# Kernel optimization log

Hardware: AMD Instinct MI355X
Metric: run time of the kernel (lower is better)

The kernel has to match this reference:

```python
import jax, jax.numpy as jnp
import numpy as np

LEAKY_SLOPE = 0.2
MASK_VAL = -9e15


def setup_inputs() -> dict:
    key = jax.random.key(0)
    k1, k2, k3, k4, k5, k6 = jax.random.split(key, 6)
    N_ex, N_kc, F_in, F_out = 20000, 1024, 128, 128
    exercise_h = jax.random.normal(k1, (N_ex, F_in), dtype=jnp.float32)
    kc_h = jax.random.normal(k2, (N_kc, F_in), dtype=jnp.float32)
    adj_exercise_kc = jax.random.randint(k3, (N_ex, N_kc), 0, 2, dtype=jnp.int32)
    # learned params (kaiming-ish scale)
    W1 = jax.random.normal(k4, (F_in, F_out), dtype=jnp.float32) * np.sqrt(2.0 / F_in)
    E = jax.random.normal(k5, (F_in, F_out), dtype=jnp.float32) * np.sqrt(2.0 / F_in)
    a = jax.random.normal(k6, (2 * F_out, 1), dtype=jnp.float32) * np.sqrt(2.0 / (2 * F_out))
    return {"exercise_h": exercise_h, "kc_h": kc_h,
            "adj_exercise_kc": adj_exercise_kc, "W1": W1, "E": E, "a": a}


def reference(exercise_h, kc_h, adj_exercise_kc, W1, E, a):
    F_out = W1.shape[1]
    kc_Wh = kc_h @ W1              # [N_kc, F_out]
    ex_Wh = exercise_h @ W1        # [N_ex, F_out]
    # Decompose a into halves: cat([ex_Wh_i, kc_Wh_j]) @ a == ex_Wh_i@a1 + kc_Wh_j@a2.
    a1, a2 = a[:F_out, 0], a[F_out:, 0]
    e = jax.nn.leaky_relu(ex_Wh @ a1[:, None] + (kc_Wh @ a2)[None, :],
                          negative_slope=LEAKY_SLOPE)   # [N_ex, N_kc]
    e = jnp.where(adj_exercise_kc > 0, e, MASK_VAL)
    attention = jax.nn.softmax(e, axis=1)
    new_kc_embed = attention @ kc_Wh               # [N_ex, F_out]
    exercise_Eh = exercise_h @ E                   # mode == 2
    return jax.nn.elu(new_kc_embed * exercise_Eh)
```

## Files before the change

### kernel.cpp

```cpp
#include <hip/hip_runtime.h>
#include <math.h>

#define N_EXC   20000
#define N_KCC   1024
#define FDIM    128
#define LEAKY_S 0.2f

#define BR  32
#define TJ  64
#define EXS 136
#define KCS 72

typedef __attribute__((ext_vector_type(8))) short short8;
typedef __attribute__((ext_vector_type(4))) float floatx4;

__device__ __forceinline__ unsigned short f2bf(float f) {
    unsigned u = __float_as_uint(f);
    u += 0x7FFF + ((u >> 16) & 1);
    return (unsigned short)(u >> 16);
}


__global__ __launch_bounds__(256) void gat_prep(const float* __restrict__ kc_h,
                                                const float* __restrict__ W1,
                                                const float* __restrict__ E,
                                                const float* __restrict__ a,
                                                float* __restrict__ ws)
{
    float* tarr = ws;
    float* w1a1 = ws + N_KCC;
    unsigned short* kcWh_t = (unsigned short*)(ws + N_KCC + FDIM);
    unsigned short* E_t    = kcWh_t + FDIM * N_KCC;
    const int tid = threadIdx.x;
    const int b = blockIdx.x;

    if (b == 128) {
        if (tid < FDIM) {
            float acc = 0.f;
            const float* row = W1 + tid * FDIM;
            #pragma unroll 8
            for (int f = 0; f < FDIM; ++f) acc += row[f] * a[f];
            w1a1[tid] = acc;
        }
        return;
    }
    if (b == 129) {
        for (int u = 0; u < 64; ++u) {
            int flat = u * 256 + tid;
            int k = flat >> 7, n = flat & 127;
            E_t[n * FDIM + k] = f2bf(E[flat]);
        }
        return;
    }

    __shared__ float kcr[8 * FDIM];
    __shared__ float red[256];
    #pragma unroll
    for (int u = 0; u < 4; ++u) {
        int flat = u * 256 + tid;
        kcr[flat] = kc_h[b * 8 * FDIM + flat];
    }
    __syncthreads();
    const int jl = tid >> 5, fg = tid & 31;
    const int j = b * 8 + jl;
    float acc0 = 0.f, acc1 = 0.f, acc2 = 0.f, acc3 = 0.f;
    #pragma unroll 4
    for (int k = 0; k < FDIM; ++k) {
        float kv = kcr[jl * FDIM + k];
        float4 w4 = *(const float4*)(W1 + k * FDIM + fg * 4);
        acc0 += kv * w4.x; acc1 += kv * w4.y; acc2 += kv * w4.z; acc3 += kv * w4.w;
    }
    kcWh_t[(fg * 4 + 0) * N_KCC + j] = f2bf(acc0);
    kcWh_t[(fg * 4 + 1) * N_KCC + j] = f2bf(acc1);
    kcWh_t[(fg * 4 + 2) * N_KCC + j] = f2bf(acc2);
    kcWh_t[(fg * 4 + 3) * N_KCC + j] = f2bf(acc3);
    float p = acc0 * a[FDIM + fg * 4 + 0] + acc1 * a[FDIM + fg * 4 + 1]
            + acc2 * a[FDIM + fg * 4 + 2] + acc3 * a[FDIM + fg * 4 + 3];
    red[tid] = p;
    __syncthreads();
    if (tid < 8) {
        float s = 0.f;
        #pragma unroll 8
        for (int l = 0; l < 32; ++l) s += red[tid * 32 + l];
        tarr[b * 8 + tid] = s;
    }
}

__global__ __launch_bounds__(256, 4) void gat_main(const float* __restrict__ ex_h,
                                                   const int* __restrict__ adj,
                                                   const float* __restrict__ ws,
                                                   float* __restrict__ out)
{
    const float* tarr = ws;
    const float* w1a1 = ws + N_KCC;
    const unsigned short* kcWh_t = (const unsigned short*)(ws + N_KCC + FDIM);
    const unsigned short* E_t    = kcWh_t + FDIM * N_KCC;

    __shared__ float t_lds[N_KCC];
    __shared__ unsigned short ex_lds[BR * EXS];
    __shared__ unsigned short kc_lds[FDIM * KCS];
    __shared__ unsigned short w_lds[BR * KCS];
    __shared__ float w1a1_lds[FDIM];
    __shared__ float scrA[256];
    __shared__ float scrB[256];
    __shared__ float s_lds[BR], m_lds[BR], denom_lds[BR];

    const int tid  = threadIdx.x;
    const int R0   = blockIdx.x * BR;
    const int lane = tid & 63, wid = tid >> 6;
    const int l15  = lane & 15, quad = lane >> 4;

    #pragma unroll
    for (int u = 0; u < 4; ++u) t_lds[u * 256 + tid] = tarr[u * 256 + tid];
    if (tid < FDIM) w1a1_lds[tid] = w1a1[tid];
    const int r0 = tid >> 3;
    const int fc = (tid & 7) * 16;
    float exv[16];
    {
        const float* src = ex_h + (size_t)(R0 + r0) * FDIM + fc;
        #pragma unroll
        for (int c = 0; c < 4; ++c) {
            float4 v = *(const float4*)(src + c * 4);
            exv[c * 4 + 0] = v.x; exv[c * 4 + 1] = v.y;
            exv[c * 4 + 2] = v.z; exv[c * 4 + 3] = v.w;
        }
        unsigned pk[8];
        #pragma unroll
        for (int i = 0; i < 8; ++i)
            pk[i] = (unsigned)f2bf(exv[2 * i]) | ((unsigned)f2bf(exv[2 * i + 1]) << 16);
        *(uint4*)(ex_lds + r0 * EXS + fc)     = make_uint4(pk[0], pk[1], pk[2], pk[3]);
        *(uint4*)(ex_lds + r0 * EXS + fc + 8) = make_uint4(pk[4], pk[5], pk[6], pk[7]);
    }
    __syncthreads();

    {
        float mx = fmaxf(fmaxf(t_lds[tid], t_lds[256 + tid]),
                         fmaxf(t_lds[512 + tid], t_lds[768 + tid]));
        scrB[tid] = mx;
        float p = 0.f;
        #pragma unroll
        for (int i = 0; i < 16; ++i) p += exv[i] * w1a1_lds[fc + i];
        scrA[tid] = p;
    }
    __syncthreads();
    if (tid < 64)
        scrB[tid] = fmaxf(fmaxf(scrB[tid], scrB[tid + 64]),
                          fmaxf(scrB[tid + 128], scrB[tid + 192]));
    __syncthreads();
    if (tid < BR) {
        float Tm = scrB[0];
        #pragma unroll 8
        for (int i = 1; i < 64; ++i) Tm = fmaxf(Tm, scrB[i]);
        float s = 0.f;
        #pragma unroll
        for (int g = 0; g < 8; ++g) s += scrA[tid * 8 + g];
        s_lds[tid] = s;
        float x = s + Tm;
        m_lds[tid] = (x >= 0.f) ? x : LEAKY_S * x;
    }

    floatx4 eh_acc[2][2], att_acc[2][2];
    #pragma unroll
    for (int mg = 0; mg < 2; ++mg)
        #pragma unroll
        for (int h = 0; h < 2; ++h) {
            eh_acc[mg][h] = (floatx4){0.f, 0.f, 0.f, 0.f};
            att_acc[mg][h] = (floatx4){0.f, 0.f, 0.f, 0.f};
        }
    #pragma unroll
    for (int h = 0; h < 2; ++h) {
        __syncthreads();
        #pragma unroll
        for (int u = 0; u < 4; ++u) {
            int flat = u * 256 + tid;
            int n = flat >> 4, kp = (flat & 15) * 8;
            *(int4*)(kc_lds + n * EXS + kp) = *(const int4*)(E_t + (h * 64 + n) * FDIM + kp);
        }
        __syncthreads();
        #pragma unroll
        for (int kk = 0; kk < 4; ++kk) {
            short8 a0 = *(const short8*)(ex_lds + (l15) * EXS + kk * 32 + quad * 8);
            short8 a1 = *(const short8*)(ex_lds + (16 + l15) * EXS + kk * 32 + quad * 8);
            short8 bf = *(const short8*)(kc_lds + (wid * 16 + l15) * EXS + kk * 32 + quad * 8);
            eh_acc[0][h] = __builtin_amdgcn_mfma_f32_16x16x32_bf16(a0, bf, eh_acc[0][h], 0, 0, 0);
            eh_acc[1][h] = __builtin_amdgcn_mfma_f32_16x16x32_bf16(a1, bf, eh_acc[1][h], 0, 0, 0);
        }
    }

    const int r_w = tid >> 3;
    const int jg  = tid & 7;
    const float sr = s_lds[r_w];
    const float mr = m_lds[r_w];
    float denom_part = 0.f;
    const int* aptr0 = adj + (size_t)(R0 + r_w) * N_KCC + jg * 8;
    int4 nx0 = *(const int4*)(aptr0);
    int4 nx1 = *(const int4*)(aptr0 + 4);

    for (int jt = 0; jt < N_KCC / TJ; ++jt) {
        const int j0 = jt * TJ;
        int4 c0 = nx0, c1 = nx1;
        __syncthreads();
        #pragma unroll
        for (int u = 0; u < 4; ++u) {
            int flat = u * 256 + tid;
            int f = flat >> 3, jp = (flat & 7) * 8;
            *(int4*)(kc_lds + f * KCS + jp) = *(const int4*)(kcWh_t + f * N_KCC + j0 + jp);
        }
        {
            int jn = (jt + 1 < N_KCC / TJ) ? (jt + 1) * TJ : jt * TJ;
            nx0 = *(const int4*)(aptr0 + jn);
            nx1 = *(const int4*)(aptr0 + jn + 4);
        }
        {
            const int jb = j0 + jg * 8;
            float4 t4a = *(const float4*)(t_lds + jb);
            float4 t4b = *(const float4*)(t_lds + jb + 4);
            float tv[8] = {t4a.x, t4a.y, t4a.z, t4a.w, t4b.x, t4b.y, t4b.z, t4b.w};
            int   av[8] = {c0.x, c0.y, c0.z, c0.w, c1.x, c1.y, c1.z, c1.w};
            unsigned pk[4];
            #pragma unroll
            for (int i = 0; i < 4; ++i) {
                float w2[2];
                #pragma unroll
                for (int e = 0; e < 2; ++e) {
                    float x = sr + tv[2 * i + e];
                    x = (x >= 0.f) ? x : LEAKY_S * x;
                    float wv = __expf(x - mr);
                    wv = (av[2 * i + e] > 0) ? wv : 0.f;
                    denom_part += wv;
                    w2[e] = wv;
                }
                pk[i] = (unsigned)f2bf(w2[0]) | ((unsigned)f2bf(w2[1]) << 16);
            }
            *(uint4*)(w_lds + r_w * KCS + jg * 8) = make_uint4(pk[0], pk[1], pk[2], pk[3]);
        }
        __syncthreads();
        #pragma unroll
        for (int kk = 0; kk < 2; ++kk) {
            short8 a0 = *(const short8*)(w_lds + (l15) * KCS + kk * 32 + quad * 8);
            short8 a1 = *(const short8*)(w_lds + (16 + l15) * KCS + kk * 32 + quad * 8);
            short8 b0 = *(const short8*)(kc_lds + ((wid) * 16 + l15) * KCS + kk * 32 + quad * 8);
            short8 b1 = *(const short8*)(kc_lds + ((4 + wid) * 16 + l15) * KCS + kk * 32 + quad * 8);
            att_acc[0][0] = __builtin_amdgcn_mfma_f32_16x16x32_bf16(a0, b0, att_acc[0][0], 0, 0, 0);
            att_acc[1][0] = __builtin_amdgcn_mfma_f32_16x16x32_bf16(a1, b0, att_acc[1][0], 0, 0, 0);
            att_acc[0][1] = __builtin_amdgcn_mfma_f32_16x16x32_bf16(a0, b1, att_acc[0][1], 0, 0, 0);
            att_acc[1][1] = __builtin_amdgcn_mfma_f32_16x16x32_bf16(a1, b1, att_acc[1][1], 0, 0, 0);
        }
    }

    __syncthreads();
    scrA[tid] = denom_part;
    __syncthreads();
    if (tid < BR) {
        float d = 0.f;
        #pragma unroll
        for (int g = 0; g < 8; ++g) d += scrA[tid * 8 + g];
        denom_lds[tid] = (d > 0.f) ? d : 1.f;
    }
    __syncthreads();

    #pragma unroll
    for (int mg = 0; mg < 2; ++mg) {
        float rd[4];
        #pragma unroll
        for (int reg = 0; reg < 4; ++reg)
            rd[reg] = 1.f / denom_lds[mg * 16 + quad * 4 + reg];
        #pragma unroll
        for (int h = 0; h < 2; ++h) {
            const int col = (h * 4 + wid) * 16 + l15;
            #pragma unroll
            for (int reg = 0; reg < 4; ++reg) {
                const int rl = mg * 16 + quad * 4 + reg;
                float v = att_acc[mg][h][reg] * rd[reg] * eh_acc[mg][h][reg];
                out[(size_t)(R0 + rl) * FDIM + col] = (v > 0.f) ? v : expm1f(v);
            }
        }
    }
}

extern "C" void kernel_launch(void* const* d_in, const int* in_sizes, int n_in,
                              void* d_out, int out_size, void* d_ws, size_t ws_size,
                              hipStream_t stream)
{
    const float* ex_h = (const float*)d_in[0];
    const float* kc_h = (const float*)d_in[1];
    const int*   adj  = (const int*)d_in[2];
    const float* W1   = (const float*)d_in[3];
    const float* E    = (const float*)d_in[4];
    const float* a    = (const float*)d_in[5];
    float* outp = (float*)d_out;
    float* ws   = (float*)d_ws;

    gat_prep<<<130, 256, 0, stream>>>(kc_h, W1, E, a, ws);
    gat_main<<<N_EXC / BR, 256, 0, stream>>>(ex_h, adj, ws, outp);
}
```

Measured before the change: 164.2 us.

## Pre-swizzle kcWh/E tiles and stream them to LDS with async loads

The prep kernel is rebuilt to emit kc_Wh and E as bf16 tiles in an XOR-swizzled layout. The main kernel then copies them straight into LDS with global_load_lds async copies instead of register round-trips, and the swizzle is meant to avoid bank conflicts without padding. The j-tile doubles to 128 so there are half as many loop iterations and barriers. Weight packing switches to a cheaper perm-based bf16 conversion, and the occupancy hint drops from 4 to 3 blocks per CU because of the larger LDS footprint. The async copy is not waited on before the barrier, so correctness depends on the compiler inserting vmcnt waits.

```diff
diff --git a/kernel.cpp b/kernel.cpp
--- a/kernel.cpp
+++ b/kernel.cpp
@@ -7,17 +7,24 @@
 #define LEAKY_S 0.2f
 
 #define BR  32
-#define TJ  64
+#define TJ  128
 #define EXS 136
-#define KCS 72
-
+
+typedef unsigned short ushort_t;
 typedef __attribute__((ext_vector_type(8))) short short8;
 typedef __attribute__((ext_vector_type(4))) float floatx4;
 
-__device__ __forceinline__ unsigned short f2bf(float f) {
+__device__ __forceinline__ ushort_t f2bf(float f) {
     unsigned u = __float_as_uint(f);
     u += 0x7FFF + ((u >> 16) & 1);
-    return (unsigned short)(u >> 16);
+    return (ushort_t)(u >> 16);
+}
+
+__device__ __forceinline__ void async16(const void* g, void* l) {
+    __builtin_amdgcn_global_load_lds(
+        (const __attribute__((address_space(1))) unsigned int*)g,
+        (__attribute__((address_space(3))) unsigned int*)l,
+        16, 0, 0);
 }
 
 
@@ -29,86 +36,142 @@
 {
     float* tarr = ws;
     float* w1a1 = ws + N_KCC;
-    unsigned short* kcWh_t = (unsigned short*)(ws + N_KCC + FDIM);
-    unsigned short* E_t    = kcWh_t + FDIM * N_KCC;
+    ushort_t* kc_sw = (ushort_t*)(ws + N_KCC + FDIM);
+    ushort_t* E_sw  = kc_sw + FDIM * N_KCC;
     const int tid = threadIdx.x;
     const int b = blockIdx.x;
 
-    if (b == 128) {
-        if (tid < FDIM) {
+    __shared__ __align__(16) float kct[128 * 132];
+    __shared__ __align__(16) ushort_t sw[32 * 128];
+    __shared__ __align__(16) float w1a2_lds[FDIM];
+
+    if (b < 32) {
+        const int jb = b >> 2, fq = b & 3;
+        const float* kcbase = kc_h + (size_t)jb * 128 * FDIM;
+        #pragma unroll
+        for (int u = 0; u < 16; ++u) {
+            int flat = u * 256 + tid;
+            int r = flat >> 5, c4 = (flat & 31) * 4;
+            float4 v = *(const float4*)(kcbase + r * FDIM + c4);
+            kct[r * 132 + c4 + 0] = v.x; kct[r * 132 + c4 + 1] = v.y;
+            kct[r * 132 + c4 + 2] = v.z; kct[r * 132 + c4 + 3] = v.w;
+        }
+        __syncthreads();
+        const int jg = tid >> 4;
+        const int fg = tid & 15;
+        const int f0 = fq * 32 + fg * 2;
+        float acc[8][2];
+        #pragma unroll
+        for (int i = 0; i < 8; ++i) { acc[i][0] = 0.f; acc[i][1] = 0.f; }
+        for (int k4 = 0; k4 < FDIM; k4 += 4) {
+            float4 av[8];
+            #pragma unroll
+            for (int i = 0; i < 8; ++i)
+                av[i] = *(const float4*)(kct + (jg * 8 + i) * 132 + k4);
+            #pragma unroll
+            for (int kk = 0; kk < 4; ++kk) {
+                float2 bv = *(const float2*)(W1 + (k4 + kk) * FDIM + f0);
+                #pragma unroll
+                for (int i = 0; i < 8; ++i) {
+                    float a_ = ((const float*)&av[i])[kk];
+                    acc[i][0] += a_ * bv.x;
+                    acc[i][1] += a_ * bv.y;
+                }
+            }
+        }
+        #pragma unroll
+        for (int c = 0; c < 2; ++c) {
+            int f = f0 + c;
+            int fl = fg * 2 + c;
+            unsigned pk[4];
+            #pragma unroll
+            for (int i = 0; i < 4; ++i)
+                pk[i] = (unsigned)f2bf(acc[2 * i][c]) | ((unsigned)f2bf(acc[2 * i + 1][c]) << 16);
+            int cp = jg ^ (f & 15);
+            *(uint4*)(sw + fl * 128 + cp * 8) = make_uint4(pk[0], pk[1], pk[2], pk[3]);
+        }
+        __syncthreads();
+        ushort_t* dst = kc_sw + ((size_t)jb * 128 + fq * 32) * 128;
+        #pragma unroll
+        for (int u = 0; u < 2; ++u) {
+            int flat = u * 256 + tid;
+            *(uint4*)(dst + flat * 8) = *(const uint4*)(sw + flat * 8);
+        }
+        return;
+    }
+
+    if (b < 36) {
+        if (tid >= 128) {
+            int k = tid - 128;
+            float acc = 0.f;
+            const float* row = W1 + k * FDIM;
+            #pragma unroll 8
+            for (int f = 0; f < FDIM; ++f) acc += row[f] * a[FDIM + f];
+            w1a2_lds[k] = acc;
+        } else if (b == 32) {
             float acc = 0.f;
             const float* row = W1 + tid * FDIM;
             #pragma unroll 8
             for (int f = 0; f < FDIM; ++f) acc += row[f] * a[f];
             w1a1[tid] = acc;
         }
-        return;
-    }
-    if (b == 129) {
-        for (int u = 0; u < 64; ++u) {
-            int flat = u * 256 + tid;
-            int k = flat >> 7, n = flat & 127;
-            E_t[n * FDIM + k] = f2bf(E[flat]);
-        }
-        return;
-    }
-
-    __shared__ float kcr[8 * FDIM];
-    __shared__ float red[256];
-    #pragma unroll
-    for (int u = 0; u < 4; ++u) {
-        int flat = u * 256 + tid;
-        kcr[flat] = kc_h[b * 8 * FDIM + flat];
-    }
-    __syncthreads();
-    const int jl = tid >> 5, fg = tid & 31;
-    const int j = b * 8 + jl;
-    float acc0 = 0.f, acc1 = 0.f, acc2 = 0.f, acc3 = 0.f;
-    #pragma unroll 4
-    for (int k = 0; k < FDIM; ++k) {
-        float kv = kcr[jl * FDIM + k];
-        float4 w4 = *(const float4*)(W1 + k * FDIM + fg * 4);
-        acc0 += kv * w4.x; acc1 += kv * w4.y; acc2 += kv * w4.z; acc3 += kv * w4.w;
-    }
-    kcWh_t[(fg * 4 + 0) * N_KCC + j] = f2bf(acc0);
-    kcWh_t[(fg * 4 + 1) * N_KCC + j] = f2bf(acc1);
-    kcWh_t[(fg * 4 + 2) * N_KCC + j] = f2bf(acc2);
-    kcWh_t[(fg * 4 + 3) * N_KCC + j] = f2bf(acc3);
-    float p = acc0 * a[FDIM + fg * 4 + 0] + acc1 * a[FDIM + fg * 4 + 1]
-            + acc2 * a[FDIM + fg * 4 + 2] + acc3 * a[FDIM + fg * 4 + 3];
-    red[tid] = p;
-    __syncthreads();
-    if (tid < 8) {
+        __syncthreads();
+        int j = (b - 32) * 256 + tid;
         float s = 0.f;
         #pragma unroll 8
-        for (int l = 0; l < 32; ++l) s += red[tid * 32 + l];
-        tarr[b * 8 + tid] = s;
-    }
-}
-
-__global__ __launch_bounds__(256, 4) void gat_main(const float* __restrict__ ex_h,
+        for (int c = 0; c < 32; ++c) {
+            float4 v = *(const float4*)(kc_h + (size_t)j * FDIM + c * 4);
+            s += v.x * w1a2_lds[c * 4 + 0] + v.y * w1a2_lds[c * 4 + 1]
+               + v.z * w1a2_lds[c * 4 + 2] + v.w * w1a2_lds[c * 4 + 3];
+        }
+        tarr[j] = s;
+        return;
+    }
+
+    #pragma unroll
+    for (int u = 0; u < 8; ++u) {
+        int ch = u * 256 + tid;
+        int n = ch >> 4, cp = ch & 15;
+        int c = cp ^ (n & 15);
+        unsigned pk[4];
+        #pragma unroll
+        for (int i = 0; i < 4; ++i) {
+            float e0 = E[(c * 8 + 2 * i + 0) * FDIM + n];
+            float e1 = E[(c * 8 + 2 * i + 1) * FDIM + n];
+            pk[i] = (unsigned)f2bf(e0) | ((unsigned)f2bf(e1) << 16);
+        }
+        *(uint4*)(E_sw + ch * 8) = make_uint4(pk[0], pk[1], pk[2], pk[3]);
+    }
+}
+
+__global__ __launch_bounds__(256, 3) void gat_main(const float* __restrict__ ex_h,
                                                    const int* __restrict__ adj,
                                                    const float* __restrict__ ws,
                                                    float* __restrict__ out)
 {
     const float* tarr = ws;
     const float* w1a1 = ws + N_KCC;
-    const unsigned short* kcWh_t = (const unsigned short*)(ws + N_KCC + FDIM);
-    const unsigned short* E_t    = kcWh_t + FDIM * N_KCC;
-
-    __shared__ float t_lds[N_KCC];
-    __shared__ unsigned short ex_lds[BR * EXS];
-    __shared__ unsigned short kc_lds[FDIM * KCS];
-    __shared__ unsigned short w_lds[BR * KCS];
+    const ushort_t* kc_sw = (const ushort_t*)(ws + N_KCC + FDIM);
+    const ushort_t* E_sw  = kc_sw + FDIM * N_KCC;
+
+    __shared__ __align__(16) float t_lds[N_KCC];
+    __shared__ __align__(16) ushort_t kc_lds[FDIM * TJ];
+    __shared__ __align__(16) ushort_t exw_lds[BR * EXS];
+    __shared__ __align__(16) float scrA[256];
+    __shared__ __align__(16) float scrB[256];
     __shared__ float w1a1_lds[FDIM];
-    __shared__ float scrA[256];
-    __shared__ float scrB[256];
     __shared__ float s_lds[BR], m_lds[BR], denom_lds[BR];
 
     const int tid  = threadIdx.x;
     const int R0   = blockIdx.x * BR;
     const int lane = tid & 63, wid = tid >> 6;
     const int l15  = lane & 15, quad = lane >> 4;
+
+    #pragma unroll
+    for (int u = 0; u < 8; ++u) {
+        int ci = u * 256 + tid;
+        async16(E_sw + ci * 8, kc_lds + ci * 8);
+    }
 
     #pragma unroll
     for (int u = 0; u < 4; ++u) t_lds[u * 256 + tid] = tarr[u * 256 + tid];
@@ -128,8 +191,8 @@
         #pragma unroll
         for (int i = 0; i < 8; ++i)
             pk[i] = (unsigned)f2bf(exv[2 * i]) | ((unsigned)f2bf(exv[2 * i + 1]) << 16);
-        *(uint4*)(ex_lds + r0 * EXS + fc)     = make_uint4(pk[0], pk[1], pk[2], pk[3]);
-        *(uint4*)(ex_lds + r0 * EXS + fc + 8) = make_uint4(pk[4], pk[5], pk[6], pk[7]);
+        *(uint4*)(exw_lds + r0 * EXS + fc)     = make_uint4(pk[0], pk[1], pk[2], pk[3]);
+        *(uint4*)(exw_lds + r0 * EXS + fc + 8) = make_uint4(pk[4], pk[5], pk[6], pk[7]);
     }
     __syncthreads();
 
@@ -158,30 +221,25 @@
         float x = s + Tm;
         m_lds[tid] = (x >= 0.f) ? x : LEAKY_S * x;
     }
+    __syncthreads();
 
     floatx4 eh_acc[2][2], att_acc[2][2];
     #pragma unroll
     for (int mg = 0; mg < 2; ++mg)
         #pragma unroll
         for (int h = 0; h < 2; ++h) {
-            eh_acc[mg][h] = (floatx4){0.f, 0.f, 0.f, 0.f};
+            eh_acc[mg][h]  = (floatx4){0.f, 0.f, 0.f, 0.f};
             att_acc[mg][h] = (floatx4){0.f, 0.f, 0.f, 0.f};
         }
     #pragma unroll
-    for (int h = 0; h < 2; ++h) {
-        __syncthreads();
-        #pragma unroll
-        for (int u = 0; u < 4; ++u) {
-            int flat = u * 256 + tid;
-            int n = flat >> 4, kp = (flat & 15) * 8;
-            *(int4*)(kc_lds + n * EXS + kp) = *(const int4*)(E_t + (h * 64 + n) * FDIM + kp);
-        }
-        __syncthreads();
-        #pragma unroll
-        for (int kk = 0; kk < 4; ++kk) {
-            short8 a0 = *(const short8*)(ex_lds + (l15) * EXS + kk * 32 + quad * 8);
-            short8 a1 = *(const short8*)(ex_lds + (16 + l15) * EXS + kk * 32 + quad * 8);
-            short8 bf = *(const short8*)(kc_lds + (wid * 16 + l15) * EXS + kk * 32 + quad * 8);
+    for (int kk = 0; kk < 4; ++kk) {
+        short8 a0 = *(const short8*)(exw_lds + l15 * EXS + kk * 32 + quad * 8);
+        short8 a1 = *(const short8*)(exw_lds + (16 + l15) * EXS + kk * 32 + quad * 8);
+        #pragma unroll
+        for (int h = 0; h < 2; ++h) {
+            const int n = (h * 4 + wid) * 16 + l15;
+            const int cp = (kk * 4 + quad) ^ l15;
+            short8 bf = *(const short8*)(kc_lds + n * TJ + cp * 8);
             eh_acc[0][h] = __builtin_amdgcn_mfma_f32_16x16x32_bf16(a0, bf, eh_acc[0][h], 0, 0, 0);
             eh_acc[1][h] = __builtin_amdgcn_mfma_f32_16x16x32_bf16(a1, bf, eh_acc[1][h], 0, 0, 0);
         }
@@ -192,59 +250,72 @@
     const float sr = s_lds[r_w];
     const float mr = m_lds[r_w];
     float denom_part = 0.f;
-    const int* aptr0 = adj + (size_t)(R0 + r_w) * N_KCC + jg * 8;
-    int4 nx0 = *(const int4*)(aptr0);
-    int4 nx1 = *(const int4*)(aptr0 + 4);
+    const int* aptr = adj + (size_t)(R0 + r_w) * N_KCC + jg * 16;
+    int4 cur0 = *(const int4*)(aptr + 0);
+    int4 cur1 = *(const int4*)(aptr + 4);
+    int4 cur2 = *(const int4*)(aptr + 8);
+    int4 cur3 = *(const int4*)(aptr + 12);
 
     for (int jt = 0; jt < N_KCC / TJ; ++jt) {
         const int j0 = jt * TJ;
-        int4 c0 = nx0, c1 = nx1;
-        __syncthreads();
-        #pragma unroll
-        for (int u = 0; u < 4; ++u) {
-            int flat = u * 256 + tid;
-            int f = flat >> 3, jp = (flat & 7) * 8;
-            *(int4*)(kc_lds + f * KCS + jp) = *(const int4*)(kcWh_t + f * N_KCC + j0 + jp);
-        }
+        __syncthreads();
+        {
+            const ushort_t* gsrc = kc_sw + (size_t)jt * (FDIM * TJ);
+            #pragma unroll
+            for (int u = 0; u < 8; ++u) {
+                int ci = u * 256 + tid;
+                async16(gsrc + ci * 8, kc_lds + ci * 8);
+            }
+        }
+        {
+            const int jb = j0 + jg * 16;
+            int av[16] = {cur0.x, cur0.y, cur0.z, cur0.w, cur1.x, cur1.y, cur1.z, cur1.w,
+                          cur2.x, cur2.y, cur2.z, cur2.w, cur3.x, cur3.y, cur3.z, cur3.w};
+            float wv[16];
+            #pragma unroll
+            for (int c = 0; c < 4; ++c) {
+                float4 t4 = *(const float4*)(t_lds + jb + c * 4);
+                float tv[4] = {t4.x, t4.y, t4.z, t4.w};
+                #pragma unroll
+                for (int e = 0; e < 4; ++e) {
+                    float x = sr + tv[e];
+                    x = fmaxf(x, LEAKY_S * x);
+                    float w = __expf(x - mr);
+                    w = (av[c * 4 + e] > 0) ? w : 0.f;
+                    denom_part += w;
+                    wv[c * 4 + e] = w;
+                }
+            }
+            unsigned pk[8];
+            #pragma unroll
+            for (int i = 0; i < 8; ++i) {
+                unsigned ua = __float_as_uint(wv[2 * i + 0]) + 0x8000u;
+                unsigned ub = __float_as_uint(wv[2 * i + 1]) + 0x8000u;
+                pk[i] = __builtin_amdgcn_perm(ub, ua, 0x07060302);
+            }
+            *(uint4*)(exw_lds + r_w * EXS + jg * 16)     = make_uint4(pk[0], pk[1], pk[2], pk[3]);
+            *(uint4*)(exw_lds + r_w * EXS + jg * 16 + 8) = make_uint4(pk[4], pk[5], pk[6], pk[7]);
+        }
+        __syncthreads();
         {
             int jn = (jt + 1 < N_KCC / TJ) ? (jt + 1) * TJ : jt * TJ;
-            nx0 = *(const int4*)(aptr0 + jn);
-            nx1 = *(const int4*)(aptr0 + jn + 4);
-        }
-        {
-            const int jb = j0 + jg * 8;
-            float4 t4a = *(const float4*)(t_lds + jb);
-            float4 t4b = *(const float4*)(t_lds + jb + 4);
-            float tv[8] = {t4a.x, t4a.y, t4a.z, t4a.w, t4b.x, t4b.y, t4b.z, t4b.w};
-            int   av[8] = {c0.x, c0.y, c0.z, c0.w, c1.x, c1.y, c1.z, c1.w};
-            unsigned pk[4];
-            #pragma unroll
-            for (int i = 0; i < 4; ++i) {
-                float w2[2];
-                #pragma unroll
-                for (int e = 0; e < 2; ++e) {
-                    float x = sr + tv[2 * i + e];
-                    x = (x >= 0.f) ? x : LEAKY_S * x;
-                    float wv = __expf(x - mr);
-                    wv = (av[2 * i + e] > 0) ? wv : 0.f;
-                    denom_part += wv;
-                    w2[e] = wv;
-                }
-                pk[i] = (unsigned)f2bf(w2[0]) | ((unsigned)f2bf(w2[1]) << 16);
-            }
-            *(uint4*)(w_lds + r_w * KCS + jg * 8) = make_uint4(pk[0], pk[1], pk[2], pk[3]);
-        }
-        __syncthreads();
-        #pragma unroll
-        for (int kk = 0; kk < 2; ++kk) {
-            short8 a0 = *(const short8*)(w_lds + (l15) * KCS + kk * 32 + quad * 8);
-            short8 a1 = *(const short8*)(w_lds + (16 + l15) * KCS + kk * 32 + quad * 8);
-            short8 b0 = *(const short8*)(kc_lds + ((wid) * 16 + l15) * KCS + kk * 32 + quad * 8);
-            short8 b1 = *(const short8*)(kc_lds + ((4 + wid) * 16 + l15) * KCS + kk * 32 + quad * 8);
-            att_acc[0][0] = __builtin_amdgcn_mfma_f32_16x16x32_bf16(a0, b0, att_acc[0][0], 0, 0, 0);
-            att_acc[1][0] = __builtin_amdgcn_mfma_f32_16x16x32_bf16(a1, b0, att_acc[1][0], 0, 0, 0);
-            att_acc[0][1] = __builtin_amdgcn_mfma_f32_16x16x32_bf16(a0, b1, att_acc[0][1], 0, 0, 0);
-            att_acc[1][1] = __builtin_amdgcn_mfma_f32_16x16x32_bf16(a1, b1, att_acc[1][1], 0, 0, 0);
+            cur0 = *(const int4*)(aptr + jn + 0);
+            cur1 = *(const int4*)(aptr + jn + 4);
+            cur2 = *(const int4*)(aptr + jn + 8);
+            cur3 = *(const int4*)(aptr + jn + 12);
+        }
+        #pragma unroll
+        for (int kk = 0; kk < 4; ++kk) {
+            short8 a0 = *(const short8*)(exw_lds + l15 * EXS + kk * 32 + quad * 8);
+            short8 a1 = *(const short8*)(exw_lds + (16 + l15) * EXS + kk * 32 + quad * 8);
+            #pragma unroll
+            for (int h = 0; h < 2; ++h) {
+                const int f = (h * 4 + wid) * 16 + l15;
+                const int cp = (kk * 4 + quad) ^ l15;
+                short8 bf = *(const short8*)(kc_lds + f * TJ + cp * 8);
+                att_acc[0][h] = __builtin_amdgcn_mfma_f32_16x16x32_bf16(a0, bf, att_acc[0][h], 0, 0, 0);
+                att_acc[1][h] = __builtin_amdgcn_mfma_f32_16x16x32_bf16(a1, bf, att_acc[1][h], 0, 0, 0);
+            }
         }
     }
 
@@ -291,6 +362,6 @@
     float* outp = (float*)d_out;
     float* ws   = (float*)d_ws;
 
-    gat_prep<<<130, 256, 0, stream>>>(kc_h, W1, E, a, ws);
+    gat_prep<<<37, 256, 0, stream>>>(kc_h, W1, E, a, ws);
     gat_main<<<N_EXC / BR, 256, 0, stream>>>(ex_h, adj, ws, outp);
 }
```

Result: faster. 158.0 us (-3.8%).
